# Performance work log

Hardware: AMD Instinct MI355X
Metric: run time of the kernel (lower is better)

The kernel has to match this reference:

```python
import jax, jax.numpy as jnp
import numpy as np
from jax.ops import segment_sum, segment_max

N_NODES, N_EDGES, D_IN, D_H, D_E, HEADS, LAYERS, D_OUT, N_GRAPHS = 50000, 150000, 48, 64, 16, 10, 3, 128, 4096


def setup_inputs() -> dict:
    key = jax.random.key(0)
    ks = jax.random.split(key, 24)
    x = jax.random.normal(ks[0], (N_NODES, D_IN), jnp.float32)
    edge_attr = jax.random.uniform(ks[1], (N_EDGES, D_E), jnp.float32)
    edge_index = jax.random.randint(ks[2], (2, N_EDGES), 0, N_NODES, dtype=jnp.int32)
    batch_ids = jnp.sort(jax.random.randint(ks[3], (N_NODES,), 0, N_GRAPHS, dtype=jnp.int32))
    s = 0.05
    W_emb = jax.random.normal(ks[4], (D_IN, D_H), jnp.float32) * s
    b_emb = jnp.zeros((D_H,), jnp.float32)
    Ws = jax.random.normal(ks[5], (LAYERS, D_H, HEADS * D_H), jnp.float32) * s
    att_src = jax.random.normal(ks[6], (LAYERS, HEADS, D_H), jnp.float32) * s
    att_dst = jax.random.normal(ks[7], (LAYERS, HEADS, D_H), jnp.float32) * s
    att_edge = jax.random.normal(ks[8], (LAYERS, HEADS, D_H), jnp.float32) * s
    W_edge = jax.random.normal(ks[9], (LAYERS, D_E, HEADS * D_H), jnp.float32) * s
    bias = jnp.zeros((LAYERS, D_H), jnp.float32)
    bn_gamma = jnp.ones((LAYERS, D_H), jnp.float32)
    bn_beta = jnp.zeros((LAYERS, D_H), jnp.float32)
    bn_mean = jax.random.normal(ks[10], (LAYERS, D_H), jnp.float32) * 0.1
    bn_var = jax.random.uniform(ks[11], (LAYERS, D_H), jnp.float32) + 0.5
    W_out = jax.random.normal(ks[12], (D_H, D_OUT), jnp.float32) * s
    b_out = jnp.zeros((D_OUT,), jnp.float32)
    return dict(x=x, edge_attr=edge_attr, W_emb=W_emb, b_emb=b_emb, Ws=Ws,
                att_src=att_src, att_dst=att_dst, att_edge=att_edge, W_edge=W_edge,
                bias=bias, bn_gamma=bn_gamma, bn_beta=bn_beta, bn_mean=bn_mean,
                bn_var=bn_var, W_out=W_out, b_out=b_out,
                edge_index=edge_index, batch_ids=batch_ids)


def reference(x, edge_attr, W_emb, b_emb, Ws, att_src, att_dst, att_edge, W_edge,
              bias, bn_gamma, bn_beta, bn_mean, bn_var, W_out, b_out,
              edge_index, batch_ids):
    N = x.shape[0]
    H, F = att_src.shape[1], att_src.shape[2]
    src, dst = edge_index[0], edge_index[1]
    # PyG add_self_loops(fill_value='mean'): self-loop edge_attr = scatter-mean of incoming edge_attr
    cnt = segment_sum(jnp.ones(src.shape, jnp.float32), dst, num_segments=N)
    loop_attr = segment_sum(edge_attr, dst, num_segments=N) / jnp.maximum(cnt, 1.0)[:, None]
    ar = jnp.arange(N, dtype=src.dtype)
    src2 = jnp.concatenate([src, ar])
    dst2 = jnp.concatenate([dst, ar])
    ea2 = jnp.concatenate([edge_attr, loop_attr], axis=0)  # [E+N, De]

    h = x @ W_emb + b_emb  # [N, D_H]
    for i in range(Ws.shape[0]):
        xp = (h @ Ws[i]).reshape(N, H, F)                       # [N,H,F]
        a_s = jnp.einsum('nhf,hf->nh', xp, att_src[i])
        a_d = jnp.einsum('nhf,hf->nh', xp, att_dst[i])
        ep = (ea2 @ W_edge[i]).reshape(-1, H, F)                # [E2,H,F]
        a_e = jnp.einsum('ehf,hf->eh', ep, att_edge[i])
        alpha = jax.nn.leaky_relu(a_s[src2] + a_d[dst2] + a_e, 0.2)  # [E2,H]
        m = segment_max(alpha, dst2, num_segments=N)            # segment softmax over dst
        e = jnp.exp(alpha - m[dst2])
        z = segment_sum(e, dst2, num_segments=N)
        att = e / z[dst2]                                       # [E2,H]
        agg = segment_sum(xp[src2] * att[:, :, None], dst2, num_segments=N)  # [N,H,F]
        xc = agg.mean(axis=1) + bias[i]                         # concat=False -> head mean
        xc = (xc - bn_mean[i]) * bn_gamma[i] / jnp.sqrt(bn_var[i] + 1e-5) + bn_beta[i]
        xc = jax.nn.gelu(xc, approximate=False)
        h = h + xc                                              # residual_connection == 'res'
    out = h @ W_out + b_out                                     # [N, D_OUT]
    gsum = segment_sum(out, batch_ids, num_segments=N_GRAPHS)
    gcnt = segment_sum(jnp.ones((N,), jnp.float32), batch_ids, num_segments=N_GRAPHS)
    return gsum / jnp.maximum(gcnt, 1.0)[:, None]               # global_mean_pool [G, D_OUT]
```

## Files before the change

kernel.cpp:

```cpp
#include <hip/hip_runtime.h>
#include <hip/hip_fp16.h>
#include <math.h>

constexpr int NN   = 50000;
constexpr int NE   = 150000;
constexpr int DIN  = 48;
constexpr int DH   = 64;
constexpr int DE   = 16;
constexpr int NHD  = 10;
constexpr int NL   = 3;
constexpr int DOUTC= 128;
constexpr int NG   = 4096;
constexpr int E2   = NE + NN;
constexpr int SCAN_B  = 256;
constexpr int SCAN_NB = (NN + SCAN_B - 1) / SCAN_B;

typedef __bf16 v8bf __attribute__((ext_vector_type(8)));
typedef short  v8s  __attribute__((ext_vector_type(8)));
typedef float  v4f  __attribute__((ext_vector_type(4)));

__device__ inline unsigned short f2bf(float f) {
    unsigned u = __builtin_bit_cast(unsigned, f);
    unsigned r = (u + 0x7FFFu + ((u >> 16) & 1u)) >> 16;
    return (unsigned short)r;
}

__device__ inline v4f MF(v8s a, v8s b, v4f c) {
    return __builtin_amdgcn_mfma_f32_16x16x32_bf16(
        __builtin_bit_cast(v8bf, a), __builtin_bit_cast(v8bf, b), c, 0, 0, 0);
}
__device__ inline v4f MFB(v8bf a, v8s b, v4f c) {
    return __builtin_amdgcn_mfma_f32_16x16x32_bf16(
        a, __builtin_bit_cast(v8bf, b), c, 0, 0, 0);
}

#define RLI(v, l) __builtin_amdgcn_readlane((v), (l))
#define RLH2(v, l) __builtin_bit_cast(__half2, __builtin_amdgcn_readlane(__builtin_bit_cast(int, (v)), (l)))

__global__ void k_zero(int* __restrict__ cnt) {
    int i = blockIdx.x * blockDim.x + threadIdx.x;
    if (i < NN) cnt[i] = 0;
}

__global__ void k_cnt(const int* __restrict__ dst, int* __restrict__ cnt) {
    int e = blockIdx.x * blockDim.x + threadIdx.x;
    if (e < NE) atomicAdd(&cnt[dst[e]], 1);
}

__global__ void k_scan_a(const int* __restrict__ cnt, int* __restrict__ bsum) {
    __shared__ int s[SCAN_B];
    int i = blockIdx.x * SCAN_B + threadIdx.x;
    s[threadIdx.x] = (i < NN) ? (cnt[i] + 1) : 0;
    __syncthreads();
    for (int off = SCAN_B / 2; off > 0; off >>= 1) {
        if (threadIdx.x < off) s[threadIdx.x] += s[threadIdx.x + off];
        __syncthreads();
    }
    if (threadIdx.x == 0) bsum[blockIdx.x] = s[0];
}

__global__ void k_scan_c(const int* __restrict__ cnt, const int* __restrict__ bsum,
                         int* __restrict__ rp, int* __restrict__ cursor) {
    __shared__ int s[SCAN_B];
    __shared__ int boff_s;
    const int t = threadIdx.x;
    int partial = (t < SCAN_NB && t < blockIdx.x) ? bsum[t] : 0;
    s[t] = partial;
    __syncthreads();
    for (int off = SCAN_B / 2; off > 0; off >>= 1) {
        if (t < off) s[t] += s[t + off];
        __syncthreads();
    }
    if (t == 0) boff_s = s[0];
    __syncthreads();
    const int boff = boff_s;
    __syncthreads();
    int i = blockIdx.x * SCAN_B + t;
    if (i < NN) cursor[i] = 0;
    int v = (i < NN) ? (cnt[i] + 1) : 0;
    s[t] = v;
    __syncthreads();
    for (int off = 1; off < SCAN_B; off <<= 1) {
        int tv = (t >= off) ? s[t - off] : 0;
        __syncthreads();
        s[t] += tv;
        __syncthreads();
    }
    if (i < NN) {
        int excl = boff + s[t] - v;
        rp[i] = excl;
        if (i == NN - 1) rp[NN] = excl + v;
    }
}

__global__ void k_csr_fill(const int* __restrict__ src, const int* __restrict__ dst,
                           const int* __restrict__ rp, int* __restrict__ cursor,
                           int* __restrict__ eidx, int* __restrict__ scsr) {
    int e = blockIdx.x * blockDim.x + threadIdx.x;
    if (e >= E2) return;
    int d  = (e < NE) ? dst[e] : (e - NE);
    int sn = (e < NE) ? src[e] : d;
    int pos = atomicAdd(&cursor[d], 1);
    int s = rp[d] + pos;
    eidx[s] = e; scsr[s] = sn;
}

__global__ void k_misc(const int* __restrict__ rp, const int* __restrict__ scsr,
                       const int* __restrict__ eidx, const int* __restrict__ cnt,
                       const float* __restrict__ ea, const int* __restrict__ batch,
                       int* __restrict__ snl12, int* __restrict__ grp,
                       float* __restrict__ loop) {
    int tid = blockIdx.x * blockDim.x + threadIdx.x;
    if (tid < NN * 16) {
        int n = tid >> 4, j = tid & 15;
        int r0 = rp[n], deg = rp[n + 1] - r0;
        int v;
        if (j < 12)      v = (j < deg) ? scsr[r0 + j] : 0;
        else if (j == 12) v = deg;
        else if (j == 13) v = r0;
        else             v = 0;
        snl12[tid] = v;
    } else if (tid < NN * 17) {
        int n = tid - NN * 16;
        int b = batch[n];
        int pb = (n == 0) ? -1 : batch[n - 1];
        for (int g = pb + 1; g <= b; ++g) grp[g] = n;
        if (n == NN - 1) for (int g = b + 1; g <= NG; ++g) grp[g] = NN;
    } else if (tid < NN * 33) {
        int t = tid - NN * 17;
        int n = t >> 4, d = t & 15;
        int r0 = rp[n], r1 = rp[n + 1];
        float s = 0.f;
        for (int q = r0; q < r1; ++q) {
            int eid = eidx[q];
            if (eid < NE) s += ea[(size_t)eid * DE + d];
        }
        int c = cnt[n];
        loop[t] = s * ((c > 1) ? (1.0f / (float)c) : 1.0f);
    }
}

constexpr int N_BTP = NL * 40960;
constexpr int N_WCB = NL * 2048;
constexpr int N_EMB = DH * 64;
constexpr int N_WET = NL * DE * NHD;
__global__ void k_prep(const float* __restrict__ Ws, const float* __restrict__ asrc,
                       const float* __restrict__ adst, const float* __restrict__ We_in,
                       const float* __restrict__ aedge, const float* __restrict__ Wemb,
                       unsigned short* __restrict__ BtP, unsigned short* __restrict__ WcB,
                       unsigned short* __restrict__ BH, unsigned short* __restrict__ BL,
                       float* __restrict__ WeT) {
    int tid = blockIdx.x * blockDim.x + threadIdx.x;
    if (tid < N_BTP) {
        int e  = tid & 7;
        int ln = (tid >> 3) & 63;
        int t  = (tid >> 9) % 20;
        int ct = (tid / 10240) & 3;
        int l  = tid / 40960;
        int f = ct * 16 + (ln & 15);
        int kidx = t * 32 + (ln >> 4) * 8 + e;
        int k = kidx / 10, q = kidx - 10 * (kidx / 10);
        float v = Ws[((size_t)l * DH + k) * 640 + q * 64 + f] * 0.1f;
        BtP[tid] = f2bf(v);
    } else if (tid < N_BTP + N_WCB) {
        int r0 = tid - N_BTP;
        int l = r0 / 2048, r = r0 % 2048;
        int tile = r / 1024, rr = r % 1024;
        int ln = rr / 16, idx = rr % 16;
        int t2 = idx / 8, e = idx % 8;
        int k = t2 * 32 + (ln >> 4) * 8 + e;
        int jc = ln & 15;
        int j = tile * 16 + jc;
        float v = 0.f;
        if (j < 20) {
            int hh = j % NHD;
            const float* a = ((j < NHD) ? asrc : adst) + (size_t)l * NHD * DH + hh * DH;
            const float* w = Ws + ((size_t)l * DH + k) * 640 + hh * DH;
            float s = 0.f;
#pragma unroll
            for (int f = 0; f < DH; ++f) s += w[f] * a[f];
            v = s;
        }
        WcB[r0] = f2bf(v);
    } else if (tid < N_BTP + N_WCB + N_EMB) {
        int r0 = tid - N_BTP - N_WCB;
        int c = r0 >> 6, k = r0 & 63;
        float v = (k < DIN) ? Wemb[(size_t)k * DH + c] : 0.f;
        __bf16 hi = (__bf16)v;
        BH[r0] = __builtin_bit_cast(unsigned short, hi);
        BL[r0] = __builtin_bit_cast(unsigned short, (__bf16)(v - (float)hi));
    } else if (tid < N_BTP + N_WCB + N_EMB + N_WET) {
        int t3 = tid - N_BTP - N_WCB - N_EMB;
        int l = t3 / 160, rr = t3 % 160;
        int hh = rr / 16, d = rr % 16;
        const float* a = aedge + (size_t)l * NHD * DH + hh * DH;
        const float* w = We_in + ((size_t)l * DE + d) * 640 + hh * DH;
        float s = 0.f;
#pragma unroll
        for (int f = 0; f < DH; ++f) s += w[f] * a[f];
        WeT[l * 160 + hh * 16 + d] = s;
    }
}

__global__ void k_ae3(const float* __restrict__ ea, const float* __restrict__ loop,
                      const float* __restrict__ WeT, const int* __restrict__ eidx,
                      __half* __restrict__ aeAll) {
    int tid = blockIdx.x * blockDim.x + threadIdx.x;
    if (tid >= NL * E2 * NHD) return;
    int l = tid / (E2 * NHD);
    int r = tid - l * (E2 * NHD);
    int s = r / NHD, h = r - (r / NHD) * NHD;
    int eid = eidx[s];
    const float* ar = (eid < NE) ? (ea + (size_t)eid * DE) : (loop + (size_t)(eid - NE) * DE);
    const float* wt = WeT + l * 160 + h * 16;
    float4 a0 = *(const float4*)(ar + 0);
    float4 a1 = *(const float4*)(ar + 4);
    float4 a2 = *(const float4*)(ar + 8);
    float4 a3 = *(const float4*)(ar + 12);
    float4 w0 = *(const float4*)(wt + 0);
    float4 w1 = *(const float4*)(wt + 4);
    float4 w2 = *(const float4*)(wt + 8);
    float4 w3 = *(const float4*)(wt + 12);
    float v = a0.x*w0.x + a0.y*w0.y + a0.z*w0.z + a0.w*w0.w
            + a1.x*w1.x + a1.y*w1.y + a1.z*w1.z + a1.w*w1.w
            + a2.x*w2.x + a2.y*w2.y + a2.z*w2.z + a2.w*w2.w
            + a3.x*w3.x + a3.y*w3.y + a3.z*w3.z + a3.w*w3.w;
    aeAll[tid] = (__half)v;
}

__global__ __launch_bounds__(256) void k_emb(const float* __restrict__ x,
        const unsigned short* __restrict__ BH, const unsigned short* __restrict__ BL,
        const float* __restrict__ bemb, const unsigned short* __restrict__ WcB,
        float* __restrict__ h, __half* __restrict__ hh, float* __restrict__ S) {
    __shared__ __align__(16) unsigned short hlb[4][16 * 72];
    const int tid = threadIdx.x;
    const int w = tid >> 6, lane = tid & 63;
    const int la = lane & 15, lb = lane >> 4;
    const int rowbase = blockIdx.x * 64 + w * 16;
    const int nA = rowbase + la;

    v8bf ah[2], al[2];
#pragma unroll
    for (int ks = 0; ks < 2; ++ks) {
        const int k0 = ks * 32 + lb * 8;
        float xv[8];
        if (nA < NN && k0 < DIN) {
            const float* xp = x + (size_t)nA * DIN + k0;
            float4 v0 = *(const float4*)xp;
            float4 v1 = *(const float4*)(xp + 4);
            xv[0]=v0.x; xv[1]=v0.y; xv[2]=v0.z; xv[3]=v0.w;
            xv[4]=v1.x; xv[5]=v1.y; xv[6]=v1.z; xv[7]=v1.w;
        } else {
#pragma unroll
            for (int e = 0; e < 8; ++e) xv[e] = 0.f;
        }
#pragma unroll
        for (int e = 0; e < 8; ++e) {
            __bf16 hi = (__bf16)xv[e];
            ah[ks][e] = hi;
            al[ks][e] = (__bf16)(xv[e] - (float)hi);
        }
    }
    v4f acc[4];
#pragma unroll
    for (int ct = 0; ct < 4; ++ct) acc[ct] = (v4f){0.f, 0.f, 0.f, 0.f};
#pragma unroll
    for (int ct = 0; ct < 4; ++ct) {
#pragma unroll
        for (int ks = 0; ks < 2; ++ks) {
            const int boff = (ct * 16 + la) * 64 + ks * 32 + lb * 8;
            v8s bh = *(const v8s*)&BH[boff];
            v8s bl = *(const v8s*)&BL[boff];
            acc[ct] = MFB(ah[ks], bh, acc[ct]);
            acc[ct] = MFB(al[ks], bh, acc[ct]);
            acc[ct] = MFB(ah[ks], bl, acc[ct]);
        }
    }
#pragma unroll
    for (int ct = 0; ct < 4; ++ct) {
        const int c = ct * 16 + la;
        const float bi = bemb[c];
#pragma unroll
        for (int r = 0; r < 4; ++r) {
            const int row = lb * 4 + r;
            const int n = rowbase + row;
            float v = acc[ct][r] + bi;
            if (n < NN) {
                h[(size_t)n * DH + c] = v;
                hh[(size_t)n * DH + c] = (__half)v;
            }
            hlb[w][row * 72 + c] = f2bf(v);
        }
    }
    __syncthreads();
    v4f s0 = {0.f,0.f,0.f,0.f}, s1 = {0.f,0.f,0.f,0.f};
#pragma unroll
    for (int t = 0; t < 2; ++t) {
        v8s av = *(const v8s*)&hlb[w][la * 72 + t * 32 + lb * 8];
        v8s b0 = *(const v8s*)&WcB[(size_t)(lane) * 16 + t * 8];
        v8s b1 = *(const v8s*)&WcB[(size_t)(64 + lane) * 16 + t * 8];
        s0 = MF(av, b0, s0);
        s1 = MF(av, b1, s1);
    }
#pragma unroll
    for (int r = 0; r < 4; ++r) {
        const int n = rowbase + lb * 4 + r;
        if (n < NN) {
            S[(size_t)n * 20 + la] = s0[r];
            if (la < 4) S[(size_t)n * 20 + 16 + la] = s1[r];
        }
    }
}

__global__ __launch_bounds__(256) void k_layer(
        const float* __restrict__ Sin, const __half* __restrict__ ae,
        __half* __restrict__ wraw,
        const int* __restrict__ snl12, const int* __restrict__ scsr,
        const float* __restrict__ hin, const __half* __restrict__ hinh,
        const unsigned short* __restrict__ BtP, const unsigned short* __restrict__ WcB,
        int do_s, float* __restrict__ Sout,
        const float* __restrict__ bias, const float* __restrict__ gam,
        const float* __restrict__ bet, const float* __restrict__ mean,
        const float* __restrict__ var, float* __restrict__ hout,
        __half* __restrict__ houth) {
    __shared__ __align__(16) unsigned short Gl[16 * 648];
    __shared__ __align__(8)  __half wL[16 * 120];

    const int tid = threadIdx.x;
    const int w = tid >> 6, lane = tid & 63;
    const int blk = blockIdx.x;
    const int nb4 = blk * 16 + w * 4;
    const unsigned* wrawu = (const unsigned*)wraw;

    const int meta = snl12[nb4 * 16 + lane];

    __half hv[4][6];
#pragma unroll
    for (int i = 0; i < 4; ++i) {
#pragma unroll
        for (int j = 0; j < 6; ++j) {
            int sv = RLI(meta, i * 16 + j);
            hv[i][j] = hinh[(size_t)sv * DH + lane];
        }
    }

    const int i0a = (lane < 48) ? (lane / 12) : 0;
    const int s0a = (lane < 48) ? (lane - i0a * 12) : 0;
    const int sn_a  = __shfl(meta, i0a * 16 + s0a);
    const int deg_a = __shfl(meta, i0a * 16 + 12);
    const int r0_a  = __shfl(meta, i0a * 16 + 13);

    if (lane < 48 && s0a < deg_a) {
        const int li = w * 4 + i0a;
        const int n  = nb4 + i0a;
        const float* sr = Sin + (size_t)sn_a * 20;
        const float* dr = Sin + (size_t)n * 20 + 10;
        const unsigned* aer = (const unsigned*)ae + (size_t)(r0_a + s0a) * 5;
        float4 t0 = *(const float4*)sr;
        float4 t1 = *(const float4*)(sr + 4);
        float2 t2 = *(const float2*)(sr + 8);
        float2 d0 = *(const float2*)(dr + 0);
        float2 d1 = *(const float2*)(dr + 2);
        float2 d2 = *(const float2*)(dr + 4);
        float2 d3 = *(const float2*)(dr + 6);
        float2 d4 = *(const float2*)(dr + 8);
        unsigned ew[5];
#pragma unroll
        for (int p = 0; p < 5; ++p) ew[p] = aer[p];
        float as_[10] = {t0.x,t0.y,t0.z,t0.w,t1.x,t1.y,t1.z,t1.w,t2.x,t2.y};
        float sd_[10] = {d0.x,d0.y,d1.x,d1.y,d2.x,d2.y,d3.x,d3.y,d4.x,d4.y};
        float* aSrow = (float*)&Gl[li * 648];
#pragma unroll
        for (int p = 0; p < 5; ++p) {
            __half2 eh = __builtin_bit_cast(__half2, ew[p]);
            float a0 = as_[2*p]   + sd_[2*p]   + __low2float(eh);
            float a1 = as_[2*p+1] + sd_[2*p+1] + __high2float(eh);
            a0 = (a0 > 0.f) ? a0 : 0.2f * a0;
            a1 = (a1 > 0.f) ? a1 : 0.2f * a1;
            float2 fp = {a0, a1};
            *(float2*)&aSrow[s0a * 10 + 2 * p] = fp;
        }
    }
    __builtin_amdgcn_wave_barrier();

    const int i0b = (lane < 40) ? (lane / 10) : 0;
    const int h_b = (lane < 40) ? (lane - i0b * 10) : 0;
    const int deg_b = __shfl(meta, i0b * 16 + 12);
    const int r0_b  = __shfl(meta, i0b * 16 + 13);

    if (lane < 40) {
        const int i0 = i0b, h = h_b;
        const int li = w * 4 + i0;
        const int n = nb4 + i0;
        const int deg = deg_b, r0 = r0_b;
        const float* aSrow = (const float*)&Gl[li * 648];
        float aL[12];
        float m = -1e30f;
#pragma unroll
        for (int s = 0; s < 12; ++s) {
            float a = -1e30f;
            if (s < deg) { a = aSrow[s * 10 + h]; m = fmaxf(m, a); }
            aL[s] = a;
        }
        if (deg > 12) {
            const float sd = Sin[(size_t)n * 20 + 10 + h];
            for (int s = 12; s < deg; ++s) {
                int sn = scsr[r0 + s];
                float a = Sin[(size_t)sn * 20 + h] + sd + (float)ae[(size_t)(r0 + s) * NHD + h];
                a = (a > 0.f) ? a : 0.2f * a;
                wraw[(size_t)(r0 + s) * NHD + h] = (__half)a;
                m = fmaxf(m, a);
            }
        }
        float z = 0.f;
#pragma unroll
        for (int s = 0; s < 12; ++s) {
            float e = (s < deg) ? __expf(aL[s] - m) : 0.f;
            aL[s] = e;
            z += e;
        }
        for (int s = 12; s < deg; ++s) {
            float e = __expf((float)wraw[(size_t)(r0 + s) * NHD + h] - m);
            wraw[(size_t)(r0 + s) * NHD + h] = (__half)e;
            z += e;
        }
        float zi = 1.f / z;
#pragma unroll
        for (int s = 0; s < 12; ++s)
            wL[li * 120 + s * 10 + h] = (__half)(aL[s] * zi);
        for (int s = 12; s < deg; ++s)
            wraw[(size_t)(r0 + s) * NHD + h] =
                (__half)((float)wraw[(size_t)(r0 + s) * NHD + h] * zi);
    }
    __builtin_amdgcn_wave_barrier();

    const unsigned* wLu = (const unsigned*)wL;
    int wfu[4];
#pragma unroll
    for (int i = 0; i < 4; ++i)
        wfu[i] = (int)wLu[(w * 4 + i) * 60 + (lane & 31)];
#pragma unroll
    for (int i = 0; i < 4; ++i) {
        const int li = w * 4 + i;
        const int deg = RLI(meta, i * 16 + 12);
        const int r0  = RLI(meta, i * 16 + 13);
        __half2 g[5];
#pragma unroll
        for (int p = 0; p < 5; ++p) g[p] = __half2{(__half)0.f, (__half)0.f};
#pragma unroll
        for (int j = 0; j < 6; ++j) {
            __half2 hvd = __half2half2(hv[i][j]);
#pragma unroll
            for (int p = 0; p < 5; ++p)
                g[p] = __hfma2(RLH2(wfu[i], j * 5 + p), hvd, g[p]);
        }
        if (deg > 6) {
            {
                int w2 = (lane < 30) ? (int)wLu[li * 60 + 30 + lane] : 0;
                __half hv2[6];
#pragma unroll
                for (int j = 0; j < 6; ++j) {
                    int sv = RLI(meta, i * 16 + 6 + j);
                    hv2[j] = hinh[(size_t)sv * DH + lane];
                }
#pragma unroll
                for (int j = 0; j < 6; ++j) {
                    __half2 hvd = __half2half2(hv2[j]);
#pragma unroll
                    for (int p = 0; p < 5; ++p)
                        g[p] = __hfma2(RLH2(w2, j * 5 + p), hvd, g[p]);
                }
            }
            for (int c0 = 12; c0 < deg; c0 += 6) {
                const int rem = deg - c0;
                int w2 = (lane < 30 && (lane / 5) < rem)
                         ? (int)wrawu[(size_t)(r0 + c0) * 5 + lane] : 0;
                int s2 = (lane < 6 && c0 + lane < deg) ? scsr[r0 + c0 + lane] : 0;
                __half hv2[6];
#pragma unroll
                for (int j = 0; j < 6; ++j) {
                    int sv = RLI(s2, j);
                    hv2[j] = hinh[(size_t)sv * DH + lane];
                }
#pragma unroll
                for (int j = 0; j < 6; ++j) {
                    __half2 hvd = __half2half2(hv2[j]);
#pragma unroll
                    for (int p = 0; p < 5; ++p)
                        g[p] = __hfma2(RLH2(w2, j * 5 + p), hvd, g[p]);
                }
            }
        }
        const int base = li * 648 + lane * 10;
#pragma unroll
        for (int p = 0; p < 5; ++p) {
            float f0 = __low2float(g[p]), f1 = __high2float(g[p]);
            unsigned u = (unsigned)f2bf(f0) | ((unsigned)f2bf(f1) << 16);
            *(unsigned*)&Gl[base + 2 * p] = u;
        }
    }
    __syncthreads();

    const int la = lane & 15, lb = lane >> 4;
    v4f acc = {0.f, 0.f, 0.f, 0.f};
    const unsigned short* bp = BtP + (size_t)w * 20 * 512;
#pragma unroll 5
    for (int t = 0; t < 20; ++t) {
        v8s av = *(const v8s*)&Gl[la * 648 + t * 32 + lb * 8];
        v8s bv = *(const v8s*)&bp[t * 512 + lane * 8];
        acc = MF(av, bv, acc);
    }
    __syncthreads();

    unsigned short* hlb = Gl;
    const int f = w * 16 + la;
    const float bi = bias[f], gm = gam[f], bt_ = bet[f], mu = mean[f];
    const float iv = rsqrtf(var[f] + 1e-5f);
#pragma unroll
    for (int r = 0; r < 4; ++r) {
        const int local = lb * 4 + r;
        const int n = blk * 16 + local;
        float hvold = hin[(size_t)n * DH + f];
        float v = acc[r] + bi;
        v = (v - mu) * gm * iv + bt_;
        v = 0.5f * v * (1.0f + erff(v * 0.70710678118654752f));
        float hnew = hvold + v;
        hout[(size_t)n * DH + f] = hnew;
        houth[(size_t)n * DH + f] = (__half)hnew;
        hlb[local * 72 + f] = f2bf(hnew);
    }

    if (do_s) {
        __syncthreads();
        if (w < 2) {
            v4f sa = {0.f, 0.f, 0.f, 0.f};
#pragma unroll
            for (int t = 0; t < 2; ++t) {
                v8s av = *(const v8s*)&hlb[la * 72 + t * 32 + lb * 8];
                v8s bv = *(const v8s*)&WcB[(size_t)(w * 64 + lane) * 16 + t * 8];
                sa = MF(av, bv, sa);
            }
#pragma unroll
            for (int r = 0; r < 4; ++r) {
                const int n = blk * 16 + lb * 4 + r;
                if (w == 0) Sout[(size_t)n * 20 + la] = sa[r];
                else if (la < 4) Sout[(size_t)n * 20 + 16 + la] = sa[r];
            }
        }
    }
}

__global__ __launch_bounds__(256) void k_gout(const float* __restrict__ h,
        const float* __restrict__ W, const float* __restrict__ b,
        const int* __restrict__ grp, float* __restrict__ out) {
    __shared__ float Wl[DH * DOUTC];
    __shared__ float hl[4][DH];
    __shared__ float cl[4];
    for (int i = threadIdx.x; i < DH * DOUTC; i += 256) Wl[i] = W[i];
    int w = threadIdx.x >> 6, lane = threadIdx.x & 63;
    int g = blockIdx.x * 4 + w;
    int r0 = grp[g], r1 = grp[g + 1];
    float s = 0.f;
    for (int n = r0; n < r1; ++n) s += h[(size_t)n * DH + lane];
    hl[w][lane] = s;
    if (lane == 0) cl[w] = (float)(r1 - r0);
    __syncthreads();
    for (int idx = threadIdx.x; idx < 4 * DOUTC; idx += 256) {
        int gi = idx >> 7, c = idx & 127;
        float cnt = cl[gi];
        float inv = 1.f / fmaxf(cnt, 1.f);
        float acc = cnt * b[c];
        const float* hr = hl[gi];
#pragma unroll 16
        for (int k = 0; k < DH; ++k) acc += hr[k] * Wl[k * DOUTC + c];
        out[(size_t)(blockIdx.x * 4 + gi) * DOUTC + c] = acc * inv;
    }
}

extern "C" void kernel_launch(void* const* d_in, const int* in_sizes, int n_in,
                              void* d_out, int out_size, void* d_ws, size_t ws_size,
                              hipStream_t stream) {
    const float* x        = (const float*)d_in[0];
    const float* edge_attr= (const float*)d_in[1];
    const float* W_emb    = (const float*)d_in[2];
    const float* b_emb    = (const float*)d_in[3];
    const float* Ws       = (const float*)d_in[4];
    const float* att_src  = (const float*)d_in[5];
    const float* att_dst  = (const float*)d_in[6];
    const float* att_edge = (const float*)d_in[7];
    const float* W_edge   = (const float*)d_in[8];
    const float* bias     = (const float*)d_in[9];
    const float* bn_gamma = (const float*)d_in[10];
    const float* bn_beta  = (const float*)d_in[11];
    const float* bn_mean  = (const float*)d_in[12];
    const float* bn_var   = (const float*)d_in[13];
    const float* W_out    = (const float*)d_in[14];
    const float* b_out    = (const float*)d_in[15];
    const int*   srcp     = (const int*)d_in[16];
    const int*   dstp     = srcp + NE;
    const int*   batch    = (const int*)d_in[17];
    float* out = (float*)d_out;

    char* wsb = (char*)d_ws;
    size_t off = 0;
    auto alloc = [&](size_t bytes) -> void* {
        void* p = (void*)(wsb + off);
        off += (bytes + 255) & ~(size_t)255;
        return p;
    };
    float*  h0    = (float*)alloc((size_t)NN * DH * 4);
    float*  h1    = (float*)alloc((size_t)NN * DH * 4);
    __half* hh0   = (__half*)alloc((size_t)NN * DH * 2);
    __half* hh1   = (__half*)alloc((size_t)NN * DH * 2);
    float*  S0    = (float*)alloc((size_t)NN * 20 * 4);
    float*  S1    = (float*)alloc((size_t)NN * 20 * 4);
    __half* wraw  = (__half*)alloc((size_t)E2 * NHD * 2);
    __half* aeAll = (__half*)alloc((size_t)NL * E2 * NHD * 2);
    float*  loop  = (float*)alloc((size_t)NN * DE * 4);
    int*    cnt   = (int*)alloc((size_t)NN * 4);
    int*    rp    = (int*)alloc((size_t)(NN + 1) * 4);
    int*    cursor= (int*)alloc((size_t)NN * 4);
    int*    eidx  = (int*)alloc((size_t)E2 * 4);
    int*    scsr  = (int*)alloc((size_t)E2 * 4);
    int*    snl12 = (int*)alloc((size_t)NN * 16 * 4);
    int*    bsum  = (int*)alloc((size_t)SCAN_NB * 4);
    int*    grp   = (int*)alloc((size_t)(NG + 1) * 4);
    float*  WeT   = (float*)alloc((size_t)NL * 160 * 4);
    unsigned short* BtP = (unsigned short*)alloc((size_t)NL * 40960 * 2);
    unsigned short* WcB = (unsigned short*)alloc((size_t)NL * 2048 * 2);
    unsigned short* BH  = (unsigned short*)alloc((size_t)DH * 64 * 2);
    unsigned short* BL  = (unsigned short*)alloc((size_t)DH * 64 * 2);

    k_zero<<<(NN + 255) / 256, 256, 0, stream>>>(cnt);
    k_cnt<<<(NE + 255) / 256, 256, 0, stream>>>(dstp, cnt);
    k_scan_a<<<SCAN_NB, SCAN_B, 0, stream>>>(cnt, bsum);
    k_scan_c<<<SCAN_NB, SCAN_B, 0, stream>>>(cnt, bsum, rp, cursor);
    k_csr_fill<<<(E2 + 255) / 256, 256, 0, stream>>>(srcp, dstp, rp, cursor, eidx, scsr);
    k_misc<<<(NN * 33 + 255) / 256, 256, 0, stream>>>(rp, scsr, eidx, cnt, edge_attr,
                                                      batch, snl12, grp, loop);

    k_prep<<<(N_BTP + N_WCB + N_EMB + N_WET + 255) / 256, 256, 0, stream>>>(
        Ws, att_src, att_dst, W_edge, att_edge, W_emb, BtP, WcB, BH, BL, WeT);
    k_ae3<<<(NL * E2 * NHD + 255) / 256, 256, 0, stream>>>(edge_attr, loop, WeT, eidx, aeAll);

    k_emb<<<(NN + 63) / 64, 256, 0, stream>>>(x, BH, BL, b_emb, WcB, h0, hh0, S0);

    float*  hb[2]  = {h0, h1};
    __half* hhb[2] = {hh0, hh1};
    float*  Sb[2]  = {S0, S1};
    for (int l = 0; l < NL; ++l) {
        float*  hin   = hb[l & 1];
        float*  hout  = hb[(l + 1) & 1];
        __half* hinh  = hhb[l & 1];
        __half* houth = hhb[(l + 1) & 1];
        float*  Sin   = Sb[l & 1];
        float*  Sout  = Sb[(l + 1) & 1];
        k_layer<<<NN / 16, 256, 0, stream>>>(
            Sin, aeAll + (size_t)l * E2 * NHD, wraw, snl12, scsr, hin, hinh,
            BtP + (size_t)l * 40960,
            WcB + (size_t)(l + 1 < NL ? l + 1 : 0) * 2048,
            (l + 1 < NL) ? 1 : 0, Sout,
            bias + l * DH, bn_gamma + l * DH, bn_beta + l * DH,
            bn_mean + l * DH, bn_var + l * DH, hout, houth);
    }
    float* hfin = hb[NL & 1];

    k_gout<<<NG / 4, 256, 0, stream>>>(hfin, W_out, b_out, grp, out);
}
```

Measured before the change: 199.2 us.

## Fold zeroing into prep, loop layers in ae3, prefetch neighbors, half pooling

Drops the separate zero kernel by having k_prep also clear the count array, and launches k_prep first. k_ae3 now loads each edge's attributes once and computes all three layers' attention-edge terms in one loop, cutting redundant gathers. k_layer prefetches the second batch of six neighbor features up front for high-degree nodes so those loads overlap earlier work, at the cost of more registers. The final pooling reads the half-precision hidden state instead of fp32, halving that read traffic at a small precision cost.

```diff
diff --git a/kernel.cpp b/kernel.cpp
--- a/kernel.cpp
+++ b/kernel.cpp
@@ -36,11 +36,6 @@
 
 #define RLI(v, l) __builtin_amdgcn_readlane((v), (l))
 #define RLH2(v, l) __builtin_bit_cast(__half2, __builtin_amdgcn_readlane(__builtin_bit_cast(int, (v)), (l)))
-
-__global__ void k_zero(int* __restrict__ cnt) {
-    int i = blockIdx.x * blockDim.x + threadIdx.x;
-    if (i < NN) cnt[i] = 0;
-}
 
 __global__ void k_cnt(const int* __restrict__ dst, int* __restrict__ cnt) {
     int e = blockIdx.x * blockDim.x + threadIdx.x;
@@ -144,12 +139,13 @@
 constexpr int N_WCB = NL * 2048;
 constexpr int N_EMB = DH * 64;
 constexpr int N_WET = NL * DE * NHD;
+constexpr int N_PRE = N_BTP + N_WCB + N_EMB + N_WET + NN;
 __global__ void k_prep(const float* __restrict__ Ws, const float* __restrict__ asrc,
                        const float* __restrict__ adst, const float* __restrict__ We_in,
                        const float* __restrict__ aedge, const float* __restrict__ Wemb,
                        unsigned short* __restrict__ BtP, unsigned short* __restrict__ WcB,
                        unsigned short* __restrict__ BH, unsigned short* __restrict__ BL,
-                       float* __restrict__ WeT) {
+                       float* __restrict__ WeT, int* __restrict__ cnt) {
     int tid = blockIdx.x * blockDim.x + threadIdx.x;
     if (tid < N_BTP) {
         int e  = tid & 7;
@@ -199,6 +195,8 @@
 #pragma unroll
         for (int f = 0; f < DH; ++f) s += w[f] * a[f];
         WeT[l * 160 + hh * 16 + d] = s;
+    } else if (tid < N_PRE) {
+        cnt[tid - (N_BTP + N_WCB + N_EMB + N_WET)] = 0;
     }
 }
 
@@ -206,26 +204,27 @@
                       const float* __restrict__ WeT, const int* __restrict__ eidx,
                       __half* __restrict__ aeAll) {
     int tid = blockIdx.x * blockDim.x + threadIdx.x;
-    if (tid >= NL * E2 * NHD) return;
-    int l = tid / (E2 * NHD);
-    int r = tid - l * (E2 * NHD);
-    int s = r / NHD, h = r - (r / NHD) * NHD;
+    if (tid >= E2 * NHD) return;
+    int s = tid / NHD, h = tid - (tid / NHD) * NHD;
     int eid = eidx[s];
     const float* ar = (eid < NE) ? (ea + (size_t)eid * DE) : (loop + (size_t)(eid - NE) * DE);
-    const float* wt = WeT + l * 160 + h * 16;
     float4 a0 = *(const float4*)(ar + 0);
     float4 a1 = *(const float4*)(ar + 4);
     float4 a2 = *(const float4*)(ar + 8);
     float4 a3 = *(const float4*)(ar + 12);
-    float4 w0 = *(const float4*)(wt + 0);
-    float4 w1 = *(const float4*)(wt + 4);
-    float4 w2 = *(const float4*)(wt + 8);
-    float4 w3 = *(const float4*)(wt + 12);
-    float v = a0.x*w0.x + a0.y*w0.y + a0.z*w0.z + a0.w*w0.w
-            + a1.x*w1.x + a1.y*w1.y + a1.z*w1.z + a1.w*w1.w
-            + a2.x*w2.x + a2.y*w2.y + a2.z*w2.z + a2.w*w2.w
-            + a3.x*w3.x + a3.y*w3.y + a3.z*w3.z + a3.w*w3.w;
-    aeAll[tid] = (__half)v;
+#pragma unroll
+    for (int l = 0; l < NL; ++l) {
+        const float* wt = WeT + l * 160 + h * 16;
+        float4 w0 = *(const float4*)(wt + 0);
+        float4 w1 = *(const float4*)(wt + 4);
+        float4 w2 = *(const float4*)(wt + 8);
+        float4 w3 = *(const float4*)(wt + 12);
+        float v = a0.x*w0.x + a0.y*w0.y + a0.z*w0.z + a0.w*w0.w
+                + a1.x*w1.x + a1.y*w1.y + a1.z*w1.z + a1.w*w1.w
+                + a2.x*w2.x + a2.y*w2.y + a2.z*w2.z + a2.w*w2.w
+                + a3.x*w3.x + a3.y*w3.y + a3.z*w3.z + a3.w*w3.w;
+        aeAll[(size_t)l * E2 * NHD + tid] = (__half)v;
+    }
 }
 
 __global__ __launch_bounds__(256) void k_emb(const float* __restrict__ x,
@@ -335,12 +334,21 @@
     const int meta = snl12[nb4 * 16 + lane];
 
     __half hv[4][6];
+    __half hv2[4][6];
 #pragma unroll
     for (int i = 0; i < 4; ++i) {
 #pragma unroll
         for (int j = 0; j < 6; ++j) {
             int sv = RLI(meta, i * 16 + j);
             hv[i][j] = hinh[(size_t)sv * DH + lane];
+        }
+        const int deg_i = RLI(meta, i * 16 + 12);
+        if (deg_i > 6) {
+#pragma unroll
+            for (int j = 0; j < 6; ++j) {
+                int sv = RLI(meta, i * 16 + 6 + j);
+                hv2[i][j] = hinh[(size_t)sv * DH + lane];
+            }
         }
     }
 
@@ -457,15 +465,9 @@
         if (deg > 6) {
             {
                 int w2 = (lane < 30) ? (int)wLu[li * 60 + 30 + lane] : 0;
-                __half hv2[6];
 #pragma unroll
                 for (int j = 0; j < 6; ++j) {
-                    int sv = RLI(meta, i * 16 + 6 + j);
-                    hv2[j] = hinh[(size_t)sv * DH + lane];
-                }
-#pragma unroll
-                for (int j = 0; j < 6; ++j) {
-                    __half2 hvd = __half2half2(hv2[j]);
+                    __half2 hvd = __half2half2(hv2[i][j]);
 #pragma unroll
                     for (int p = 0; p < 5; ++p)
                         g[p] = __hfma2(RLH2(w2, j * 5 + p), hvd, g[p]);
@@ -476,15 +478,15 @@
                 int w2 = (lane < 30 && (lane / 5) < rem)
                          ? (int)wrawu[(size_t)(r0 + c0) * 5 + lane] : 0;
                 int s2 = (lane < 6 && c0 + lane < deg) ? scsr[r0 + c0 + lane] : 0;
-                __half hv2[6];
+                __half hv3[6];
 #pragma unroll
                 for (int j = 0; j < 6; ++j) {
                     int sv = RLI(s2, j);
-                    hv2[j] = hinh[(size_t)sv * DH + lane];
+                    hv3[j] = hinh[(size_t)sv * DH + lane];
                 }
 #pragma unroll
                 for (int j = 0; j < 6; ++j) {
-                    __half2 hvd = __half2half2(hv2[j]);
+                    __half2 hvd = __half2half2(hv3[j]);
 #pragma unroll
                     for (int p = 0; p < 5; ++p)
                         g[p] = __hfma2(RLH2(w2, j * 5 + p), hvd, g[p]);
@@ -550,7 +552,7 @@
     }
 }
 
-__global__ __launch_bounds__(256) void k_gout(const float* __restrict__ h,
+__global__ __launch_bounds__(256) void k_gout(const __half* __restrict__ hh,
         const float* __restrict__ W, const float* __restrict__ b,
         const int* __restrict__ grp, float* __restrict__ out) {
     __shared__ float Wl[DH * DOUTC];
@@ -561,7 +563,7 @@
     int g = blockIdx.x * 4 + w;
     int r0 = grp[g], r1 = grp[g + 1];
     float s = 0.f;
-    for (int n = r0; n < r1; ++n) s += h[(size_t)n * DH + lane];
+    for (int n = r0; n < r1; ++n) s += (float)hh[(size_t)n * DH + lane];
     hl[w][lane] = s;
     if (lane == 0) cl[w] = (float)(r1 - r0);
     __syncthreads();
@@ -631,7 +633,9 @@
     unsigned short* BH  = (unsigned short*)alloc((size_t)DH * 64 * 2);
     unsigned short* BL  = (unsigned short*)alloc((size_t)DH * 64 * 2);
 
-    k_zero<<<(NN + 255) / 256, 256, 0, stream>>>(cnt);
+    k_prep<<<(N_PRE + 255) / 256, 256, 0, stream>>>(
+        Ws, att_src, att_dst, W_edge, att_edge, W_emb, BtP, WcB, BH, BL, WeT, cnt);
+
     k_cnt<<<(NE + 255) / 256, 256, 0, stream>>>(dstp, cnt);
     k_scan_a<<<SCAN_NB, SCAN_B, 0, stream>>>(cnt, bsum);
     k_scan_c<<<SCAN_NB, SCAN_B, 0, stream>>>(cnt, bsum, rp, cursor);
@@ -639,9 +643,7 @@
     k_misc<<<(NN * 33 + 255) / 256, 256, 0, stream>>>(rp, scsr, eidx, cnt, edge_attr,
                                                       batch, snl12, grp, loop);
 
-    k_prep<<<(N_BTP + N_WCB + N_EMB + N_WET + 255) / 256, 256, 0, stream>>>(
-        Ws, att_src, att_dst, W_edge, att_edge, W_emb, BtP, WcB, BH, BL, WeT);
-    k_ae3<<<(NL * E2 * NHD + 255) / 256, 256, 0, stream>>>(edge_attr, loop, WeT, eidx, aeAll);
+    k_ae3<<<(E2 * NHD + 255) / 256, 256, 0, stream>>>(edge_attr, loop, WeT, eidx, aeAll);
 
     k_emb<<<(NN + 63) / 64, 256, 0, stream>>>(x, BH, BL, b_emb, WcB, h0, hh0, S0);
 
@@ -663,7 +665,7 @@
             bias + l * DH, bn_gamma + l * DH, bn_beta + l * DH,
             bn_mean + l * DH, bn_var + l * DH, hout, houth);
     }
-    float* hfin = hb[NL & 1];
-
-    k_gout<<<NG / 4, 256, 0, stream>>>(hfin, W_out, b_out, grp, out);
-}
+    __half* hfinh = hhb[NL & 1];
+
+    k_gout<<<NG / 4, 256, 0, stream>>>(hfinh, W_out, b_out, grp, out);
+}
```

Result: faster. 194.8 us (-2.2%).
